# Kernel optimization log

Measured on AMD Instinct MI355X. Metric: run time of the kernel, lower is better.

Reference implementation:

```python
import jax, jax.numpy as jnp
import numpy as np

N, D = 8192, 1024
NUM_CLASSES = 200
NUM_BATCHES = 128  # stands in for len(train_loader)


def setup_inputs() -> dict:
    key = jax.random.key(0)
    k1, k2, k3, k4 = jax.random.split(key, 4)
    return {
        "reconstructed_image_features": jax.random.normal(k1, (N, D), dtype=jnp.float32),
        "semantic_embeddings": jax.random.normal(k2, (N, D), dtype=jnp.float32),
        "residual_output": jax.random.normal(k3, (N, D), dtype=jnp.float32),
        "labels": jax.random.randint(k4, (N,), 0, NUM_CLASSES, dtype=jnp.int64),
    }


def reference(reconstructed_image_features, semantic_embeddings, residual_output, labels):
    # Normalize rows -> pairwise cosine similarity via one Gram matmul.
    z = semantic_embeddings
    eps = 1e-8  # matches torch CosineSimilarity eps
    zn = z / jnp.maximum(jnp.linalg.norm(z, axis=1, keepdims=True), eps)
    S = zn @ zn.T                      # [N, N] cosine similarities
    E = jnp.exp(S)                     # exp(cos_sim) for every pair

    same = labels[:, None] == labels[None, :]          # same-class mask
    offdiag = ~jnp.eye(S.shape[0], dtype=bool)         # torch.equal skip == skip i==j

    row_same = jnp.sum(jnp.where(same & offdiag, E, 0.0), axis=1)  # [N]
    row_diff = jnp.sum(jnp.where(~same, E, 0.0), axis=1)           # [N]

    seg_same = jax.ops.segment_sum(row_same, labels, num_segments=NUM_CLASSES)
    seg_diff = jax.ops.segment_sum(row_diff, labels, num_segments=NUM_CLASSES)
    counts = jax.ops.segment_sum(jnp.ones_like(row_same), labels, num_segments=NUM_CLASSES)

    present = counts > 0  # original only iterates over labels present in the batch
    safe_same = jnp.where(present, seg_same, 1.0)
    safe_diff = jnp.where(present, seg_diff, 1.0)
    per_label = jnp.where(present, jnp.log(safe_same / safe_diff), 0.0)

    return jnp.sum(per_label) / NUM_BATCHES
```

## Files before the change

kernel.cpp:

```cpp
#include <hip/hip_runtime.h>
#include <hip/hip_bf16.h>
#include <stdint.h>

#define N_ROWS 8192
#define DIM 1024
#define NUM_CLS 200
#define BM 256
#define BK 32
#define NT2 32
#define NSUP 10
#define GRID_BLOCKS (NSUP * 64)

typedef __attribute__((ext_vector_type(8))) short bf16x8;
typedef __attribute__((ext_vector_type(4))) float f32x4;

__device__ __forceinline__ ushort f2bf(float f) {
    __hip_bfloat16 h = __float2bfloat16(f);
    return *reinterpret_cast<ushort*>(&h);
}

__global__ __launch_bounds__(256) void normalize_kernel(const float* __restrict__ z,
                                                        ushort* __restrict__ zn) {
    const int row = blockIdx.x * 4 + (threadIdx.x >> 6);
    const int lane = threadIdx.x & 63;
    const float4 v = reinterpret_cast<const float4*>(z + (size_t)row * DIM)[lane];
    float ss = v.x * v.x + v.y * v.y + v.z * v.z + v.w * v.w;
    #pragma unroll
    for (int off = 1; off < 64; off <<= 1) ss += __shfl_xor(ss, off);
    const float inv = 1.0f / fmaxf(sqrtf(ss), 1e-8f);
    ushort4 o;
    o.x = f2bf(v.x * inv);
    o.y = f2bf(v.y * inv);
    o.z = f2bf(v.z * inv);
    o.w = f2bf(v.w * inv);
    reinterpret_cast<ushort4*>(zn + (size_t)row * DIM)[lane] = o;
}

__global__ __launch_bounds__(512, 1) void gram_kernel(const ushort* __restrict__ zn,
                                                      const int* __restrict__ labels,
                                                      float* __restrict__ row_same,
                                                      float* __restrict__ row_diff) {
    constexpr int SBi[NSUP] = {0, 0, 1, 0, 1, 2, 0, 1, 2, 3};
    constexpr int SBj[NSUP] = {0, 1, 1, 2, 2, 2, 3, 3, 3, 3};

    const int st = blockIdx.x >> 6;
    const int p = blockIdx.x & 63;
    const int xcd = p & 7;
    const int idx = p >> 3;
    const int bi_l = (xcd & 3) * 2 + (idx >> 2);
    const int bj_l = (xcd >> 2) * 4 + (idx & 3);
    const int bi = SBi[st] * 8 + bi_l;
    const int bj = SBj[st] * 8 + bj_l;
    if (bi > bj) return;
    const bool diag = (bi == bj);

    const int r0 = bi * BM, c0 = bj * BM;
    const int t = threadIdx.x;
    const int lane = t & 63, wv = t >> 6;
    const int wr = wv >> 2, wc = wv & 3;

    __shared__ ushort sA[2][BM * BK];
    __shared__ ushort sB[2][BM * BK];

    f32x4 acc[8][4];
    #pragma unroll
    for (int m = 0; m < 8; m++)
        #pragma unroll
        for (int n = 0; n < 4; n++) acc[m][n] = (f32x4){0.f, 0.f, 0.f, 0.f};

    auto stage = [&](int buf, int kt) {
        #pragma unroll
        for (int h = 0; h < 2; h++) {
            const int c = h * 512 + t;
            const int r = c >> 2;
            const int sp = c & 3;
            const int rr = (r + (r >> 2)) & 3;
            const int s = (sp - rr) & 3;
            const ushort* gA = zn + (size_t)(r0 + r) * DIM + kt + s * 8;
            __builtin_amdgcn_global_load_lds(
                (const __attribute__((address_space(1))) uint32_t*)gA,
                (__attribute__((address_space(3))) uint32_t*)&sA[buf][c * 8],
                16, 0, 0);
            const ushort* gB = zn + (size_t)(c0 + r) * DIM + kt + s * 8;
            __builtin_amdgcn_global_load_lds(
                (const __attribute__((address_space(1))) uint32_t*)gB,
                (__attribute__((address_space(3))) uint32_t*)&sB[buf][c * 8],
                16, 0, 0);
        }
    };

    stage(0, 0);
    __syncthreads();

    int cur = 0;
    const int rbase = wr * 128 + (lane & 15);
    const int cbase = wc * 64 + (lane & 15);
    const int sidx = lane >> 4;

    for (int it = 0; it < DIM / BK; ++it) {
        if (it < DIM / BK - 1) stage(cur ^ 1, (it + 1) * BK);

        bf16x8 a[4], b[4];
        #pragma unroll
        for (int x = 0; x < 4; x++) {
            const int row = rbase + x * 16;
            const int sp = (sidx + row + (row >> 2)) & 3;
            a[x] = *reinterpret_cast<const bf16x8*>(&sA[cur][row * 32 + sp * 8]);
            const int rowb = cbase + x * 16;
            const int spb = (sidx + rowb + (rowb >> 2)) & 3;
            b[x] = *reinterpret_cast<const bf16x8*>(&sB[cur][rowb * 32 + spb * 8]);
        }
        __builtin_amdgcn_s_setprio(1);
        #pragma unroll
        for (int m = 0; m < 4; m++)
            #pragma unroll
            for (int n = 0; n < 4; n++)
                acc[m][n] = __builtin_amdgcn_mfma_f32_16x16x32_bf16(
                    a[m], b[n], acc[m][n], 0, 0, 0);
        __builtin_amdgcn_s_setprio(0);

        #pragma unroll
        for (int x = 0; x < 4; x++) {
            const int row = rbase + (x + 4) * 16;
            const int sp = (sidx + row + (row >> 2)) & 3;
            a[x] = *reinterpret_cast<const bf16x8*>(&sA[cur][row * 32 + sp * 8]);
        }
        __builtin_amdgcn_s_setprio(1);
        #pragma unroll
        for (int m = 0; m < 4; m++)
            #pragma unroll
            for (int n = 0; n < 4; n++)
                acc[m + 4][n] = __builtin_amdgcn_mfma_f32_16x16x32_bf16(
                    a[m], b[n], acc[m + 4][n], 0, 0, 0);
        __builtin_amdgcn_s_setprio(0);

        __syncthreads();
        cur ^= 1;
    }

    int* labR = (int*)&sA[0][0];
    int* labC = labR + 256;
    if (t < 256) labR[t] = labels[r0 + t];
    else labC[t - 256] = labels[c0 + (t - 256)];
    __syncthreads();

    float cs[4] = {0.f, 0.f, 0.f, 0.f}, cd[4] = {0.f, 0.f, 0.f, 0.f};
    #pragma unroll
    for (int m = 0; m < 8; m++) {
        #pragma unroll
        for (int q = 0; q < 4; q++) {
            const int ii = wr * 128 + m * 16 + (lane >> 4) * 4 + q;
            const int li = labR[ii];
            float vs = 0.f, vd = 0.f;
            #pragma unroll
            for (int n = 0; n < 4; n++) {
                const int jj = wc * 64 + n * 16 + (lane & 15);
                const float e = __expf(acc[m][n][q]);
                const bool same = (li == labC[jj]);
                if (!diag || ii != jj) {
                    if (same) { vs += e; if (!diag) cs[n] += e; }
                    else      { vd += e; if (!diag) cd[n] += e; }
                }
            }
            #pragma unroll
            for (int off = 1; off < 16; off <<= 1) {
                vs += __shfl_xor(vs, off);
                vd += __shfl_xor(vd, off);
            }
            if ((lane & 15) == 0) {
                atomicAdd(&row_same[r0 + ii], vs);
                atomicAdd(&row_diff[r0 + ii], vd);
            }
        }
    }

    if (!diag) {
        #pragma unroll
        for (int n = 0; n < 4; n++) {
            float vs = cs[n], vd = cd[n];
            vs += __shfl_xor(vs, 16); vd += __shfl_xor(vd, 16);
            vs += __shfl_xor(vs, 32); vd += __shfl_xor(vd, 32);
            if (lane < 16) {
                const int j = c0 + wc * 64 + n * 16 + lane;
                atomicAdd(&row_same[j], vs);
                atomicAdd(&row_diff[j], vd);
            }
        }
    }
}

__global__ __launch_bounds__(256) void class_sum_kernel(const int* __restrict__ labels,
                                                        const float* __restrict__ row_same,
                                                        const float* __restrict__ row_diff,
                                                        float* __restrict__ cls_same,
                                                        float* __restrict__ cls_diff,
                                                        int* __restrict__ cls_cnt) {
    __shared__ float ls[NUM_CLS], ld_[NUM_CLS];
    __shared__ int lc[NUM_CLS];
    const int t = threadIdx.x;
    for (int c = t; c < NUM_CLS; c += 256) { ls[c] = 0.f; ld_[c] = 0.f; lc[c] = 0; }
    __syncthreads();
    const int r = blockIdx.x * 256 + t;
    if (r < N_ROWS) {
        const int l = labels[r];
        atomicAdd(&ls[l], row_same[r]);
        atomicAdd(&ld_[l], row_diff[r]);
        atomicAdd(&lc[l], 1);
    }
    __syncthreads();
    for (int c = t; c < NUM_CLS; c += 256) {
        if (lc[c] > 0) {
            atomicAdd(&cls_same[c], ls[c]);
            atomicAdd(&cls_diff[c], ld_[c]);
            atomicAdd(&cls_cnt[c], lc[c]);
        }
    }
}

__global__ __launch_bounds__(256) void final_kernel(const float* __restrict__ cls_same,
                                                    const float* __restrict__ cls_diff,
                                                    const int* __restrict__ cls_cnt,
                                                    float* __restrict__ out) {
    const int t = threadIdx.x;
    float p = 0.f;
    if (t < NUM_CLS && cls_cnt[t] > 0) p = logf(cls_same[t] / cls_diff[t]);
    #pragma unroll
    for (int off = 1; off < 64; off <<= 1) p += __shfl_xor(p, off);
    __shared__ float wsum[4];
    if ((t & 63) == 0) wsum[t >> 6] = p;
    __syncthreads();
    if (t == 0) out[0] = (wsum[0] + wsum[1] + wsum[2] + wsum[3]) / 128.0f;
}

extern "C" void kernel_launch(void* const* d_in, const int* in_sizes, int n_in,
                              void* d_out, int out_size, void* d_ws, size_t ws_size,
                              hipStream_t stream) {
    const float* z = (const float*)d_in[1];
    const int* labels = (const int*)d_in[3];

    ushort* zn = (ushort*)d_ws;
    char* p = (char*)d_ws + (size_t)N_ROWS * DIM * 2;
    float* row_same = (float*)p;                 p += N_ROWS * sizeof(float);
    float* row_diff = (float*)p;                 p += N_ROWS * sizeof(float);
    float* cls_same = (float*)p;                 p += 256 * sizeof(float);
    float* cls_diff = (float*)p;                 p += 256 * sizeof(float);
    int*   cls_cnt  = (int*)p;

    hipMemsetAsync(row_same, 0,
                   (2 * N_ROWS + 2 * 256) * sizeof(float) + 256 * sizeof(int),
                   stream);

    normalize_kernel<<<N_ROWS / 4, 256, 0, stream>>>(z, zn);

    gram_kernel<<<GRID_BLOCKS, 512, 0, stream>>>(zn, labels, row_same, row_diff);

    class_sum_kernel<<<N_ROWS / 256, 256, 0, stream>>>(labels, row_same, row_diff,
                                                       cls_same, cls_diff, cls_cnt);
    final_kernel<<<1, 256, 0, stream>>>(cls_same, cls_diff, cls_cnt, (float*)d_out);
}
```

Measured before the change: 266.8 us.

## Triple-buffer LDS staging with explicit vmcnt waits and compact triangular grid

Switches the Gram kernel's K-loop from double to triple buffering. Loads are issued two steps ahead and each step waits only until the oldest stage's loads retire (s_waitcnt vmcnt) before a raw barrier, instead of a full __syncthreads. It also replaces the XCD-aware supertile block mapping with a linear upper-triangular enumeration, so no blocks launch only to exit. The gains are deeper latency hiding and no wasted blocks, at the cost of 50% more LDS and the loss of the L2/XCD locality the old mapping provided.

```diff
diff --git a/kernel.cpp b/kernel.cpp
--- a/kernel.cpp
+++ b/kernel.cpp
@@ -7,9 +7,9 @@
 #define NUM_CLS 200
 #define BM 256
 #define BK 32
+#define NSTEPS (DIM / BK)
 #define NT2 32
-#define NSUP 10
-#define GRID_BLOCKS (NSUP * 64)
+#define GRID_BLOCKS (NT2 * (NT2 + 1) / 2)
 
 typedef __attribute__((ext_vector_type(8))) short bf16x8;
 typedef __attribute__((ext_vector_type(4))) float f32x4;
@@ -40,18 +40,9 @@
                                                       const int* __restrict__ labels,
                                                       float* __restrict__ row_same,
                                                       float* __restrict__ row_diff) {
-    constexpr int SBi[NSUP] = {0, 0, 1, 0, 1, 2, 0, 1, 2, 3};
-    constexpr int SBj[NSUP] = {0, 1, 1, 2, 2, 2, 3, 3, 3, 3};
-
-    const int st = blockIdx.x >> 6;
-    const int p = blockIdx.x & 63;
-    const int xcd = p & 7;
-    const int idx = p >> 3;
-    const int bi_l = (xcd & 3) * 2 + (idx >> 2);
-    const int bj_l = (xcd >> 2) * 4 + (idx & 3);
-    const int bi = SBi[st] * 8 + bi_l;
-    const int bj = SBj[st] * 8 + bj_l;
-    if (bi > bj) return;
+    int rem = blockIdx.x, bi = 0, len = NT2;
+    while (rem >= len) { rem -= len; ++bi; --len; }
+    const int bj = bi + rem;
     const bool diag = (bi == bj);
 
     const int r0 = bi * BM, c0 = bj * BM;
@@ -59,8 +50,8 @@
     const int lane = t & 63, wv = t >> 6;
     const int wr = wv >> 2, wc = wv & 3;
 
-    __shared__ ushort sA[2][BM * BK];
-    __shared__ ushort sB[2][BM * BK];
+    __shared__ ushort sA[3][BM * BK];
+    __shared__ ushort sB[3][BM * BK];
 
     f32x4 acc[8][4];
     #pragma unroll
@@ -89,26 +80,31 @@
         }
     };
 
-    stage(0, 0);
-    __syncthreads();
-
-    int cur = 0;
     const int rbase = wr * 128 + (lane & 15);
     const int cbase = wc * 64 + (lane & 15);
     const int sidx = lane >> 4;
 
-    for (int it = 0; it < DIM / BK; ++it) {
-        if (it < DIM / BK - 1) stage(cur ^ 1, (it + 1) * BK);
-
+    stage(0, 0);
+    stage(1, BK);
+    asm volatile("s_waitcnt vmcnt(4)" ::: "memory");
+    __builtin_amdgcn_s_barrier();
+    __builtin_amdgcn_sched_barrier(0);
+
+    for (int it = 0; it < NSTEPS; ++it) {
+        const int slot = it % 3;
+        if (it + 2 < NSTEPS) stage((it + 2) % 3, (it + 2) * BK);
+
+        const ushort* __restrict__ pA = sA[slot];
+        const ushort* __restrict__ pB = sB[slot];
         bf16x8 a[4], b[4];
         #pragma unroll
         for (int x = 0; x < 4; x++) {
             const int row = rbase + x * 16;
             const int sp = (sidx + row + (row >> 2)) & 3;
-            a[x] = *reinterpret_cast<const bf16x8*>(&sA[cur][row * 32 + sp * 8]);
+            a[x] = *reinterpret_cast<const bf16x8*>(&pA[row * 32 + sp * 8]);
             const int rowb = cbase + x * 16;
             const int spb = (sidx + rowb + (rowb >> 2)) & 3;
-            b[x] = *reinterpret_cast<const bf16x8*>(&sB[cur][rowb * 32 + spb * 8]);
+            b[x] = *reinterpret_cast<const bf16x8*>(&pB[rowb * 32 + spb * 8]);
         }
         __builtin_amdgcn_s_setprio(1);
         #pragma unroll
@@ -123,7 +119,7 @@
         for (int x = 0; x < 4; x++) {
             const int row = rbase + (x + 4) * 16;
             const int sp = (sidx + row + (row >> 2)) & 3;
-            a[x] = *reinterpret_cast<const bf16x8*>(&sA[cur][row * 32 + sp * 8]);
+            a[x] = *reinterpret_cast<const bf16x8*>(&pA[row * 32 + sp * 8]);
         }
         __builtin_amdgcn_s_setprio(1);
         #pragma unroll
@@ -134,14 +130,21 @@
                     a[m], b[n], acc[m + 4][n], 0, 0, 0);
         __builtin_amdgcn_s_setprio(0);
 
-        __syncthreads();
-        cur ^= 1;
-    }
+        if (it + 2 < NSTEPS) {
+            asm volatile("s_waitcnt vmcnt(4)" ::: "memory");
+        } else if (it + 1 < NSTEPS) {
+            asm volatile("s_waitcnt vmcnt(0)" ::: "memory");
+        }
+        __builtin_amdgcn_s_barrier();
+        __builtin_amdgcn_sched_barrier(0);
+    }
+
+    __syncthreads();
 
     int* labR = (int*)&sA[0][0];
     int* labC = labR + 256;
     if (t < 256) labR[t] = labels[r0 + t];
-    else labC[t - 256] = labels[c0 + (t - 256)];
+    else if (t < 512) labC[t - 256] = labels[c0 + (t - 256)];
     __syncthreads();
 
     float cs[4] = {0.f, 0.f, 0.f, 0.f}, cd[4] = {0.f, 0.f, 0.f, 0.f};
```

After: 271.6 us. No clear change (+1.8%).

## Restructure GEMM main loop into BK=64 four-phase pipeline with region-wise prefetch

Applied to the files above, without the earlier changes.

Doubles the K tile to 64 and splits each K step into four MFMA phases, each computing a quadrant of the accumulator tile. Global-to-LDS loads are issued per half-matrix region and interleaved between phases, with explicit vmcnt/lgkmcnt waits and raw s_barrier calls in place of __syncthreads. The goal is to halve the number of K iterations and overlap memory traffic with MFMA work more finely. It uses a larger LDS buffer and relies on hand-managed wait counts, which are error-prone.

```diff
diff --git a/kernel.cpp b/kernel.cpp
--- a/kernel.cpp
+++ b/kernel.cpp
@@ -6,7 +6,8 @@
 #define DIM 1024
 #define NUM_CLS 200
 #define BM 256
-#define BK 32
+#define BK 64
+#define NKT (DIM / BK)
 #define NT2 32
 #define NSUP 10
 #define GRID_BLOCKS (NSUP * 64)
@@ -58,9 +59,10 @@
     const int t = threadIdx.x;
     const int lane = t & 63, wv = t >> 6;
     const int wr = wv >> 2, wc = wv & 3;
-
-    __shared__ ushort sA[2][BM * BK];
-    __shared__ ushort sB[2][BM * BK];
+    const int lrow = lane & 15;
+    const int lgrp = lane >> 4;
+
+    __shared__ ushort lds[2 * 2 * 256 * 64];
 
     f32x4 acc[8][4];
     #pragma unroll
@@ -68,80 +70,140 @@
         #pragma unroll
         for (int n = 0; n < 4; n++) acc[m][n] = (f32x4){0.f, 0.f, 0.f, 0.f};
 
-    auto stage = [&](int buf, int kt) {
-        #pragma unroll
-        for (int h = 0; h < 2; h++) {
-            const int c = h * 512 + t;
-            const int r = c >> 2;
-            const int sp = c & 3;
-            const int rr = (r + (r >> 2)) & 3;
-            const int s = (sp - rr) & 3;
-            const ushort* gA = zn + (size_t)(r0 + r) * DIM + kt + s * 8;
+    auto stage = [&](int kt, int region) {
+        const int buf = kt & 1;
+        const int mat = (region >= 2) ? 0 : 1;
+        const int half = region & 1;
+        const size_t grow = (size_t)((mat == 0 ? r0 : c0) + half * 128);
+        ushort* ldst = &lds[(size_t)((buf * 2 + mat) * 256 + half * 128) * 64];
+        #pragma unroll
+        for (int hh = 0; hh < 2; hh++) {
+            const int c = hh * 512 + t;
+            const int r = c >> 3;
+            const int sp = c & 7;
+            const int s = (sp - r - (r >> 3)) & 7;
+            const ushort* g = zn + (grow + r) * DIM + kt * BK + s * 8;
             __builtin_amdgcn_global_load_lds(
-                (const __attribute__((address_space(1))) uint32_t*)gA,
-                (__attribute__((address_space(3))) uint32_t*)&sA[buf][c * 8],
+                (const __attribute__((address_space(1))) uint32_t*)g,
+                (__attribute__((address_space(3))) uint32_t*)&ldst[(size_t)c * 8],
                 16, 0, 0);
-            const ushort* gB = zn + (size_t)(c0 + r) * DIM + kt + s * 8;
-            __builtin_amdgcn_global_load_lds(
-                (const __attribute__((address_space(1))) uint32_t*)gB,
-                (__attribute__((address_space(3))) uint32_t*)&sB[buf][c * 8],
-                16, 0, 0);
         }
     };
 
-    stage(0, 0);
-    __syncthreads();
-
-    int cur = 0;
-    const int rbase = wr * 128 + (lane & 15);
-    const int cbase = wc * 64 + (lane & 15);
-    const int sidx = lane >> 4;
-
-    for (int it = 0; it < DIM / BK; ++it) {
-        if (it < DIM / BK - 1) stage(cur ^ 1, (it + 1) * BK);
-
-        bf16x8 a[4], b[4];
-        #pragma unroll
-        for (int x = 0; x < 4; x++) {
-            const int row = rbase + x * 16;
-            const int sp = (sidx + row + (row >> 2)) & 3;
-            a[x] = *reinterpret_cast<const bf16x8*>(&sA[cur][row * 32 + sp * 8]);
-            const int rowb = cbase + x * 16;
-            const int spb = (sidx + rowb + (rowb >> 2)) & 3;
-            b[x] = *reinterpret_cast<const bf16x8*>(&sB[cur][rowb * 32 + spb * 8]);
-        }
+    #pragma unroll
+    for (int kt = 0; kt < 2; kt++)
+        #pragma unroll
+        for (int rg = 0; rg < 4; rg++) stage(kt, rg);
+    asm volatile("s_waitcnt vmcnt(8)" ::: "memory");
+    __builtin_amdgcn_s_barrier();
+
+    bf16x8 a[4][2], b[4][2];
+
+    for (int kc = 0; kc < NKT; ++kc) {
+        const int buf = kc & 1;
+        const ushort* pA = &lds[(size_t)(buf * 2 + 0) * 256 * 64];
+        const ushort* pB = &lds[(size_t)(buf * 2 + 1) * 256 * 64];
+
+        auto rd = [&](const ushort* pM, int R, int ks) -> bf16x8 {
+            const int r = R & 127;
+            const int sp = ((ks * 4 + lgrp) + r + (r >> 3)) & 7;
+            return *reinterpret_cast<const bf16x8*>(&pM[R * 64 + sp * 8]);
+        };
+
+        #pragma unroll
+        for (int m = 0; m < 4; m++) {
+            a[m][0] = rd(pA, wr * 128 + m * 16 + lrow, 0);
+            a[m][1] = rd(pA, wr * 128 + m * 16 + lrow, 1);
+        }
+        #pragma unroll
+        for (int n = 0; n < 2; n++) {
+            b[n][0] = rd(pB, wc * 64 + n * 16 + lrow, 0);
+            b[n][1] = rd(pB, wc * 64 + n * 16 + lrow, 1);
+        }
+        if (kc >= 1 && kc <= 14) stage(kc + 1, 2);
+        __builtin_amdgcn_s_barrier();
+        asm volatile("s_waitcnt lgkmcnt(0)" ::: "memory");
+        __builtin_amdgcn_sched_barrier(0);
         __builtin_amdgcn_s_setprio(1);
         #pragma unroll
         for (int m = 0; m < 4; m++)
             #pragma unroll
-            for (int n = 0; n < 4; n++)
-                acc[m][n] = __builtin_amdgcn_mfma_f32_16x16x32_bf16(
-                    a[m], b[n], acc[m][n], 0, 0, 0);
+            for (int n = 0; n < 2; n++)
+                #pragma unroll
+                for (int ks = 0; ks < 2; ks++)
+                    acc[m][n] = __builtin_amdgcn_mfma_f32_16x16x32_bf16(
+                        a[m][ks], b[n][ks], acc[m][n], 0, 0, 0);
         __builtin_amdgcn_s_setprio(0);
-
-        #pragma unroll
-        for (int x = 0; x < 4; x++) {
-            const int row = rbase + (x + 4) * 16;
-            const int sp = (sidx + row + (row >> 2)) & 3;
-            a[x] = *reinterpret_cast<const bf16x8*>(&sA[cur][row * 32 + sp * 8]);
-        }
+        __builtin_amdgcn_s_barrier();
+
+        #pragma unroll
+        for (int n = 2; n < 4; n++) {
+            b[n][0] = rd(pB, wc * 64 + n * 16 + lrow, 0);
+            b[n][1] = rd(pB, wc * 64 + n * 16 + lrow, 1);
+        }
+        if (kc >= 1 && kc <= 14) stage(kc + 1, 3);
+        __builtin_amdgcn_s_barrier();
+        asm volatile("s_waitcnt lgkmcnt(0)" ::: "memory");
+        __builtin_amdgcn_sched_barrier(0);
         __builtin_amdgcn_s_setprio(1);
         #pragma unroll
         for (int m = 0; m < 4; m++)
             #pragma unroll
-            for (int n = 0; n < 4; n++)
-                acc[m + 4][n] = __builtin_amdgcn_mfma_f32_16x16x32_bf16(
-                    a[m], b[n], acc[m + 4][n], 0, 0, 0);
+            for (int n = 2; n < 4; n++)
+                #pragma unroll
+                for (int ks = 0; ks < 2; ks++)
+                    acc[m][n] = __builtin_amdgcn_mfma_f32_16x16x32_bf16(
+                        a[m][ks], b[n][ks], acc[m][n], 0, 0, 0);
         __builtin_amdgcn_s_setprio(0);
-
-        __syncthreads();
-        cur ^= 1;
-    }
-
-    int* labR = (int*)&sA[0][0];
+        __builtin_amdgcn_s_barrier();
+
+        #pragma unroll
+        for (int m = 0; m < 4; m++) {
+            a[m][0] = rd(pA, wr * 128 + (m + 4) * 16 + lrow, 0);
+            a[m][1] = rd(pA, wr * 128 + (m + 4) * 16 + lrow, 1);
+        }
+        if (kc <= 13) stage(kc + 2, 0);
+        __builtin_amdgcn_s_barrier();
+        asm volatile("s_waitcnt lgkmcnt(0)" ::: "memory");
+        __builtin_amdgcn_sched_barrier(0);
+        __builtin_amdgcn_s_setprio(1);
+        #pragma unroll
+        for (int m = 0; m < 4; m++)
+            #pragma unroll
+            for (int n = 0; n < 2; n++)
+                #pragma unroll
+                for (int ks = 0; ks < 2; ks++)
+                    acc[m + 4][n] = __builtin_amdgcn_mfma_f32_16x16x32_bf16(
+                        a[m][ks], b[n][ks], acc[m + 4][n], 0, 0, 0);
+        __builtin_amdgcn_s_setprio(0);
+        __builtin_amdgcn_s_barrier();
+
+        if (kc <= 13) stage(kc + 2, 1);
+        __builtin_amdgcn_s_barrier();
+        __builtin_amdgcn_s_setprio(1);
+        #pragma unroll
+        for (int m = 0; m < 4; m++)
+            #pragma unroll
+            for (int n = 2; n < 4; n++)
+                #pragma unroll
+                for (int ks = 0; ks < 2; ks++)
+                    acc[m + 4][n] = __builtin_amdgcn_mfma_f32_16x16x32_bf16(
+                        a[m][ks], b[n][ks], acc[m + 4][n], 0, 0, 0);
+        __builtin_amdgcn_s_setprio(0);
+        if (kc <= 13) {
+            asm volatile("s_waitcnt vmcnt(4)" ::: "memory");
+        } else if (kc == 14) {
+            asm volatile("s_waitcnt vmcnt(0)" ::: "memory");
+        }
+        __builtin_amdgcn_s_barrier();
+    }
+
+    __syncthreads();
+
+    int* labR = (int*)&lds[0];
     int* labC = labR + 256;
     if (t < 256) labR[t] = labels[r0 + t];
-    else labC[t - 256] = labels[c0 + (t - 256)];
+    else if (t < 512) labC[t - 256] = labels[c0 + (t - 256)];
     __syncthreads();
 
     float cs[4] = {0.f, 0.f, 0.f, 0.f}, cd[4] = {0.f, 0.f, 0.f, 0.f};
```

Result: faster. 257.2 us (-3.6%).
